# Optimization experiments

Hardware: AMD Instinct MI355X
Metric: run time of the kernel (lower is better)

Reference implementation:

```python
import jax, jax.numpy as jnp
import numpy as np

NUM_HEADS = 16
NUM_GQA_GROUPS = 4
HEAD_DIM = 128
TOTAL_TOKENS = 4096
NUM_SEQS = 8
SCALE = HEAD_DIM ** -0.5


def setup_inputs() -> dict:
    key = jax.random.key(0)
    kq, kk, kv, kc = jax.random.split(key, 4)
    query = jax.random.normal(kq, (TOTAL_TOKENS, NUM_HEADS, HEAD_DIM), dtype=jnp.float32)
    k = jax.random.normal(kk, (TOTAL_TOKENS, NUM_GQA_GROUPS, HEAD_DIM), dtype=jnp.float32)
    v = jax.random.normal(kv, (TOTAL_TOKENS, NUM_GQA_GROUPS, HEAD_DIM), dtype=jnp.float32)
    # cu_seqlens: sorted prefix boundaries, pinned to 0 and TOTAL_TOKENS
    inner = jnp.sort(jax.random.randint(kc, (NUM_SEQS - 1,), 1, TOTAL_TOKENS, dtype=jnp.int32))
    cu_seqlens = jnp.concatenate([
        jnp.zeros((1,), jnp.int32), inner,
        jnp.full((1,), TOTAL_TOKENS, jnp.int32)])
    return {"query": query, "key": k, "value": v, "cu_seqlens": cu_seqlens}


def reference(query, key, value, cu_seqlens):
    """Packed varlen (thd) causal attention with GQA, fused via a segment mask.

    query: [T, H, D]; key/value: [T, G, D]; cu_seqlens: [B+1] int32.
    Returns [T, H, D] (same layout the torch thd path concatenates back to).
    """
    T, H, D = query.shape
    ratio = H // key.shape[1]
    if ratio > 1:  # GQA: repeat kv heads to match query heads
        key = jnp.repeat(key, ratio, axis=1)
        value = jnp.repeat(value, ratio, axis=1)

    pos = jnp.arange(T, dtype=jnp.int32)
    # segment id of each packed token: cu[j] <= i < cu[j+1]
    seg = jnp.searchsorted(cu_seqlens, pos, side="right") - 1
    # within-segment causal mask (global causal == local causal inside a segment)
    mask = (seg[:, None] == seg[None, :]) & (pos[:, None] >= pos[None, :])  # [T, T]

    scores = jnp.einsum("qhd,khd->hqk", query, key) * SCALE  # [H, T, T]
    scores = jnp.where(mask[None], scores, -jnp.inf)
    probs = jax.nn.softmax(scores, axis=-1)
    out = jnp.einsum("hqk,khd->qhd", probs, value)  # [T, H, D]
    return out
```

## Files before the change

kernel.cpp:

```cpp
#include <hip/hip_runtime.h>
#include <hip/hip_bf16.h>


#define T_TOK 4096
#define NH    16
#define NG    4
#define HD    128
#define NCU   9
#define NTILE 128

#define ML_OFF  33554432l
#define Q_OFF   34078720l
#define KBF_OFF 34080776l
#define VTB_OFF 35129352l
#define QBF_OFF 36177928l
#define WS_END  40372232l

typedef short          short8_t __attribute__((ext_vector_type(8)));
typedef float          float4_t __attribute__((ext_vector_type(4)));
typedef unsigned int   uint2_t  __attribute__((ext_vector_type(2)));
typedef unsigned short ushort;

static __device__ inline unsigned pack2(float a, float b) {
    __hip_bfloat162 h = __float22bfloat162_rn(make_float2(a, b));
    union { __hip_bfloat162 h; unsigned u; } c; c.h = h;
    return c.u;
}
static __device__ inline short8_t cvt8(float4_t lo, float4_t hi) {
    union { unsigned u[4]; short8_t s; } r;
    r.u[0] = pack2(lo[0], lo[1]); r.u[1] = pack2(lo[2], lo[3]);
    r.u[2] = pack2(hi[0], hi[1]); r.u[3] = pack2(hi[2], hi[3]);
    return r.s;
}

#define NPQ 4194304l
#define NPK 1048576l
__global__ __launch_bounds__(256) void prep_cvt(
    const float* __restrict__ Q, const float* __restrict__ K,
    const float* __restrict__ V, float* __restrict__ WS)
{
    unsigned* Qb  = (unsigned*)(WS + QBF_OFF);
    unsigned* Kb  = (unsigned*)(WS + KBF_OFF);
    ushort*   Vtb = (ushort*)(WS + VTB_OFF);
    const int b = (int)blockIdx.x, tid = (int)threadIdx.x;
    if (b < 2048) {
        long p = (long)b * 256 + tid;
        const long stride = 2048l * 256;
        for (; p < NPQ + NPK; p += stride) {
            if (p < NPQ) {
                const float2 v = *(const float2*)&Q[2 * p];
                Qb[p] = pack2(v.x, v.y);
            } else {
                const float2 v = *(const float2*)&K[2 * (p - NPQ)];
                Kb[p - NPQ] = pack2(v.x, v.y);
            }
        }
    } else {
        const int bt  = b - 2048;
        const int g   = bt >> 8;
        const int rem = bt & 255;
        const int d0  = (rem >> 6) * 32;
        const int t0  = (rem & 63) * 64;
        __shared__ ushort tile[64][36];
        const int i2 = tid >> 3, jl = (tid & 7) * 4;
        #pragma unroll
        for (int ii = 0; ii < 2; ++ii) {
            const int t = t0 + i2 + ii * 32;
            const float4_t v = *(const float4_t*)&V[((long)t * NG + g) * HD + d0 + jl];
            *(unsigned*)&tile[i2 + ii * 32][jl]     = pack2(v[0], v[1]);
            *(unsigned*)&tile[i2 + ii * 32][jl + 2] = pack2(v[2], v[3]);
        }
        __syncthreads();
        const int jj = tid >> 3, tl = (tid & 7) * 8;
        union { ushort s[8]; short8_t v; } o;
        #pragma unroll
        for (int r = 0; r < 8; ++r) o.s[r] = tile[tl + r][jj];
        *(short8_t*)&Vtb[((long)(g * HD + d0 + jj)) * T_TOK + t0 + tl] = o.v;
    }
}

template <int MODE>
static __device__ __forceinline__ void attn_tile_body(
    const float* __restrict__ Q, const float* __restrict__ K,
    const float* __restrict__ V,
    const ushort* __restrict__ Qb, const ushort* __restrict__ Kb,
    const ushort* __restrict__ Vtb,
    const int* __restrict__ cu,
    float* __restrict__ O, float* __restrict__ WS,
    unsigned char* smem, int qtile, int g, int cz)
{
    constexpr bool CHUNKED = (MODE >= 1);
    constexpr bool BF      = (MODE == 2);

    ushort (*Ks)[32][136]   = (ushort (*)[32][136])smem;
    ushort (*Vt)[128][40]   = (ushort (*)[128][40])(smem + 17408);
    ushort (*pb)[2][16][40] = (ushort (*)[2][16][40])(smem + 37888);

    const int tid   = threadIdx.x;
    const int wave  = tid >> 6;
    const int split = wave >> 2;
    const int hw    = wave & 3;
    const int lane  = tid & 63;
    const int h     = g * 4 + hw;
    const int col   = lane & 15;
    const int quad  = lane >> 4;

    const int qbase = qtile * 32;
    const int qq[2] = { qbase + col, qbase + 16 + col };

    int seg_start[2] = {0, 0}, seg0 = 0;
    #pragma unroll
    for (int j = 1; j < NCU; ++j) {
        int cj = cu[j];
        if (cj <= qq[0])  seg_start[0] = cj;
        if (cj <= qq[1])  seg_start[1] = cj;
        if (cj <= qbase)  seg0         = cj;
    }
    const int k0       = seg0 & ~31;
    const int nblk_tot = (qbase + 32 - k0) >> 5;
    const int nc       = CHUNKED ? ((nblk_tot + 31) >> 5) : 1;
    if (CHUNKED && cz >= nc) return;
    int nblk = nblk_tot - (cz << 5);
    if (CHUNKED && nblk > 32) nblk = 32;
    const int nb0    = (nblk + 1) >> 1;
    const int kstart = k0 + (cz << 10) + split * nb0 * 32;

    const int smax[2] = { __shfl(seg_start[0], 15), __shfl(seg_start[1], 15) };

    short8_t qf[2][4];
    #pragma unroll
    for (int tt = 0; tt < 2; ++tt) {
        if constexpr (BF) {
            const ushort* qp = Qb + ((long)qq[tt] * NH + h) * HD + quad * 8;
            #pragma unroll
            for (int c = 0; c < 4; ++c)
                qf[tt][c] = *(const short8_t*)(qp + c * 32);
        } else {
            const float* qp = Q + ((long)qq[tt] * NH + h) * HD + quad * 8;
            #pragma unroll
            for (int c = 0; c < 4; ++c)
                qf[tt][c] = cvt8(*(const float4_t*)(qp + c * 32),
                                 *(const float4_t*)(qp + c * 32 + 4));
        }
    }

    float4_t oacc[2][8];
    #pragma unroll
    for (int tt = 0; tt < 2; ++tt)
        #pragma unroll
        for (int dt = 0; dt < 8; ++dt) oacc[tt][dt] = (float4_t){0.f, 0.f, 0.f, 0.f};

    float m_run[2] = {-10000.0f, -10000.0f};
    float l_run[2] = {0.0f, 0.0f};
    const float c_scale = 0.08838834764831845f * 1.4426950408889634f;

    const int stid = tid & 255;
    const int ki  = stid >> 3;
    const int ch  = (stid & 7) * 16;
    const int kp2 = (stid & 15) * 2;
    const int dc  = (stid >> 4) * 8;
    const int vd  = stid >> 1;
    const int vko = (stid & 1) * 16;

    float4_t kreg[4], vreg[4];
    short8_t krb[2], vrb[2];
    if constexpr (BF) {
        int key = kstart + ki; if (key > T_TOK - 1) key = T_TOK - 1;
        const ushort* kp = Kb + ((long)key * NG + g) * HD + ch;
        krb[0] = *(const short8_t*)kp; krb[1] = *(const short8_t*)(kp + 8);
        int ts = kstart + vko; if (ts > T_TOK - 16) ts = T_TOK - 16;
        const ushort* vp = Vtb + ((long)(g * HD + vd)) * T_TOK + ts;
        vrb[0] = *(const short8_t*)vp; vrb[1] = *(const short8_t*)(vp + 8);
    } else {
        int key = kstart + ki; if (key > T_TOK - 1) key = T_TOK - 1;
        const float* kp = K + ((long)key * NG + g) * HD + ch;
        kreg[0] = *(const float4_t*)kp;       kreg[1] = *(const float4_t*)(kp + 4);
        kreg[2] = *(const float4_t*)(kp + 8); kreg[3] = *(const float4_t*)(kp + 12);
        int key0 = kstart + kp2;     if (key0 > T_TOK - 1) key0 = T_TOK - 1;
        int key1 = kstart + kp2 + 1; if (key1 > T_TOK - 1) key1 = T_TOK - 1;
        const float* v0 = V + ((long)key0 * NG + g) * HD + dc;
        const float* v1 = V + ((long)key1 * NG + g) * HD + dc;
        vreg[0] = *(const float4_t*)v0; vreg[1] = *(const float4_t*)(v0 + 4);
        vreg[2] = *(const float4_t*)v1; vreg[3] = *(const float4_t*)(v1 + 4);
    }

    for (int it = 0; it < nb0; ++it) {
        const int kb = kstart + it * 32;
        __syncthreads();

        if constexpr (BF) {
            *(short8_t*)&Ks[split][ki][ch]      = krb[0];
            *(short8_t*)&Ks[split][ki][ch + 8]  = krb[1];
            *(short8_t*)&Vt[split][vd][vko]     = vrb[0];
            *(short8_t*)&Vt[split][vd][vko + 8] = vrb[1];
        } else {
            *(short8_t*)&Ks[split][ki][ch]     = cvt8(kreg[0], kreg[1]);
            *(short8_t*)&Ks[split][ki][ch + 8] = cvt8(kreg[2], kreg[3]);
            #pragma unroll
            for (int d = 0; d < 4; ++d) {
                *(unsigned*)&Vt[split][dc + d][kp2]     = pack2(vreg[0][d], vreg[2][d]);
                *(unsigned*)&Vt[split][dc + 4 + d][kp2] = pack2(vreg[1][d], vreg[3][d]);
            }
        }
        __syncthreads();

        {
            int nb = kb + 32;
            if constexpr (BF) {
                int key = nb + ki; if (key > T_TOK - 1) key = T_TOK - 1;
                const ushort* kp = Kb + ((long)key * NG + g) * HD + ch;
                krb[0] = *(const short8_t*)kp; krb[1] = *(const short8_t*)(kp + 8);
                int ts = nb + vko; if (ts > T_TOK - 16) ts = T_TOK - 16;
                const ushort* vp = Vtb + ((long)(g * HD + vd)) * T_TOK + ts;
                vrb[0] = *(const short8_t*)vp; vrb[1] = *(const short8_t*)(vp + 8);
            } else {
                int key = nb + ki; if (key > T_TOK - 1) key = T_TOK - 1;
                const float* kp = K + ((long)key * NG + g) * HD + ch;
                kreg[0] = *(const float4_t*)kp;       kreg[1] = *(const float4_t*)(kp + 4);
                kreg[2] = *(const float4_t*)(kp + 8); kreg[3] = *(const float4_t*)(kp + 12);
                int key0 = nb + kp2;     if (key0 > T_TOK - 1) key0 = T_TOK - 1;
                int key1 = nb + kp2 + 1; if (key1 > T_TOK - 1) key1 = T_TOK - 1;
                const float* v0 = V + ((long)key0 * NG + g) * HD + dc;
                const float* v1 = V + ((long)key1 * NG + g) * HD + dc;
                vreg[0] = *(const float4_t*)v0; vreg[1] = *(const float4_t*)(v0 + 4);
                vreg[2] = *(const float4_t*)v1; vreg[3] = *(const float4_t*)(v1 + 4);
            }
        }

        float4_t st[2][2];
        #pragma unroll
        for (int tt = 0; tt < 2; ++tt)
            #pragma unroll
            for (int t = 0; t < 2; ++t) st[tt][t] = (float4_t){0.f, 0.f, 0.f, 0.f};
        #pragma unroll
        for (int c = 0; c < 4; ++c) {
            short8_t kf0 = *(const short8_t*)&Ks[split][col][c * 32 + quad * 8];
            short8_t kf1 = *(const short8_t*)&Ks[split][16 + col][c * 32 + quad * 8];
            st[0][0] = __builtin_amdgcn_mfma_f32_16x16x32_bf16(kf0, qf[0][c], st[0][0], 0, 0, 0);
            st[0][1] = __builtin_amdgcn_mfma_f32_16x16x32_bf16(kf1, qf[0][c], st[0][1], 0, 0, 0);
            st[1][0] = __builtin_amdgcn_mfma_f32_16x16x32_bf16(kf0, qf[1][c], st[1][0], 0, 0, 0);
            st[1][1] = __builtin_amdgcn_mfma_f32_16x16x32_bf16(kf1, qf[1][c], st[1][1], 0, 0, 0);
        }

        #pragma unroll
        for (int tt = 0; tt < 2; ++tt) {
            float tv[8];
            if (kb + 31 <= qbase + 16 * tt && kb >= smax[tt]) {
                #pragma unroll
                for (int i = 0; i < 8; ++i)
                    tv[i] = st[tt][i >> 2][i & 3] * c_scale;
            } else {
                #pragma unroll
                for (int t = 0; t < 2; ++t)
                    #pragma unroll
                    for (int r = 0; r < 4; ++r) {
                        int key = kb + 16 * t + quad * 4 + r;
                        bool valid = (key <= qq[tt]) && (key >= seg_start[tt]);
                        tv[t * 4 + r] = valid ? st[tt][t][r] * c_scale : -30000.0f;
                    }
            }
            float tmax = tv[0];
            #pragma unroll
            for (int i = 1; i < 8; ++i) tmax = fmaxf(tmax, tv[i]);
            tmax = fmaxf(tmax, __shfl_xor(tmax, 16));
            tmax = fmaxf(tmax, __shfl_xor(tmax, 32));
            const float m_new = fmaxf(m_run[tt], tmax);
            float p[8], ps = 0.f;
            #pragma unroll
            for (int i = 0; i < 8; ++i) { p[i] = __builtin_exp2f(tv[i] - m_new); ps += p[i]; }
            ps += __shfl_xor(ps, 16);
            ps += __shfl_xor(ps, 32);
            if (__any(tmax > m_run[tt])) {
                const float alpha = __builtin_exp2f(m_run[tt] - m_new);
                l_run[tt] = l_run[tt] * alpha + ps;
                m_run[tt] = m_new;
                #pragma unroll
                for (int dt = 0; dt < 8; ++dt) oacc[tt][dt] *= alpha;
            } else {
                l_run[tt] += ps;
            }

            uint2_t w0; w0.x = pack2(p[0], p[1]); w0.y = pack2(p[2], p[3]);
            uint2_t w1; w1.x = pack2(p[4], p[5]); w1.y = pack2(p[6], p[7]);
            *(uint2_t*)&pb[wave][tt][col][quad * 4]      = w0;
            *(uint2_t*)&pb[wave][tt][col][16 + quad * 4] = w1;
        }
        short8_t pf0 = *(const short8_t*)&pb[wave][0][col][quad * 8];
        short8_t pf1 = *(const short8_t*)&pb[wave][1][col][quad * 8];

        #pragma unroll
        for (int dt = 0; dt < 8; ++dt) {
            short8_t vf = *(const short8_t*)&Vt[split][dt * 16 + col][quad * 8];
            oacc[0][dt] = __builtin_amdgcn_mfma_f32_16x16x32_bf16(vf, pf0, oacc[0][dt], 0, 0, 0);
            oacc[1][dt] = __builtin_amdgcn_mfma_f32_16x16x32_bf16(vf, pf1, oacc[1][dt], 0, 0, 0);
        }
    }

    float* Ob = (float*)smem;
    float* cm = (float*)(smem + 34816);
    float* cl = (float*)(smem + 35840);
    #pragma unroll
    for (int tt = 0; tt < 2; ++tt) {
        __syncthreads();
        if (split == 1) {
            if (quad == 0) { cm[hw * 16 + col] = m_run[tt]; cl[hw * 16 + col] = l_run[tt]; }
            float* ob = Ob + (hw * 16 + col) * 132;
            #pragma unroll
            for (int dt = 0; dt < 8; ++dt)
                *(float4_t*)(ob + dt * 16 + quad * 4) = oacc[tt][dt];
        }
        __syncthreads();
        if (split == 0) {
            const float m1 = cm[hw * 16 + col], l1 = cl[hw * 16 + col];
            const float m  = fmaxf(m_run[tt], m1);
            const float a0 = __builtin_exp2f(m_run[tt] - m);
            const float a1 = __builtin_exp2f(m1 - m);
            const float* ob = Ob + (hw * 16 + col) * 132;
            #pragma unroll
            for (int dt = 0; dt < 8; ++dt) {
                float4_t o1 = *(const float4_t*)(ob + dt * 16 + quad * 4);
                oacc[tt][dt] = oacc[tt][dt] * a0 + o1 * a1;
            }
            l_run[tt] = l_run[tt] * a0 + l1 * a1;
            m_run[tt] = m;
        }
    }

    if (split == 0) {
        if (!CHUNKED || nc == 1) {
            #pragma unroll
            for (int tt = 0; tt < 2; ++tt) {
                const float inv_l = 1.0f / l_run[tt];
                float* op = O + ((long)qq[tt] * NH + h) * HD + quad * 4;
                #pragma unroll
                for (int dt = 0; dt < 8; ++dt) {
                    float4_t ov;
                    #pragma unroll
                    for (int r = 0; r < 4; ++r) ov[r] = oacc[tt][dt][r] * inv_l;
                    *(float4_t*)(op + dt * 16) = ov;
                }
            }
        } else {
            const long slot = ((long)(qtile * 4 + g)) * 4 + cz;
            #pragma unroll
            for (int tt = 0; tt < 2; ++tt) {
                const int ql = tt * 16 + col;
                if (quad == 0) {
                    float* mlp = WS + ML_OFF + (slot * 128 + hw * 32 + ql) * 2;
                    mlp[0] = m_run[tt];
                    mlp[1] = l_run[tt];
                }
                float* op = WS + (slot * 128 + hw * 32 + ql) * 128 + quad * 4;
                #pragma unroll
                for (int dt = 0; dt < 8; ++dt)
                    *(float4_t*)(op + dt * 16) = oacc[tt][dt];
            }
        }
    }
}

__global__ __launch_bounds__(128) void build_queue(
    const int* __restrict__ cu, int* __restrict__ qwork)
{
    __shared__ int nblk_s[NTILE];
    __shared__ int sortedE[NTILE + 1];
    const int t = threadIdx.x;

    const int qbase = t * 32;
    int seg0 = 0;
    #pragma unroll
    for (int j = 1; j < NCU; ++j) { int cj = cu[j]; if (cj <= qbase) seg0 = cj; }
    const int k0   = seg0 & ~31;
    const int nblk = (qbase + 32 - k0) >> 5;
    nblk_s[t] = nblk;
    __syncthreads();

    int r = 0;
    for (int j = 0; j < NTILE; ++j) {
        int nj = nblk_s[j];
        if (nj > nblk || (nj == nblk && j < t)) ++r;
    }
    const int nc = (nblk + 31) >> 5;
    sortedE[r] = 4 * nc;
    __syncthreads();
    if (t == 0) {
        int s = 0;
        for (int j = 0; j < NTILE; ++j) { int v = sortedE[j]; sortedE[j] = s; s += v; }
        sortedE[NTILE] = s;
        qwork[0] = s;
        qwork[1] = 0;
    }
    __syncthreads();
    int off = 2 + sortedE[r];
    for (int g = 0; g < NG; ++g)
        for (int cz = 0; cz < nc; ++cz)
            qwork[off++] = (t << 4) | (g << 2) | cz;
}

template <int MODE>
__global__ __launch_bounds__(512) void attn_fwd_persist(
    const float* __restrict__ Q,
    const float* __restrict__ K,
    const float* __restrict__ V,
    const int*   __restrict__ cu,
    float*       __restrict__ O,
    float*       __restrict__ WS)
{
    __shared__ __align__(16) unsigned char smem[58368];
    __shared__ int pop_s;
    int* qwork = (int*)(WS + Q_OFF);
    const ushort* Qb  = (const ushort*)(WS + QBF_OFF);
    const ushort* Kb  = (const ushort*)(WS + KBF_OFF);
    const ushort* Vtb = (const ushort*)(WS + VTB_OFF);
    const int qtotal = qwork[0];

    for (;;) {
        __syncthreads();
        if (threadIdx.x == 0) pop_s = atomicAdd(&qwork[1], 1);
        __syncthreads();
        const int idx = pop_s;
        if (idx >= qtotal) return;
        const int ent = qwork[2 + idx];
        attn_tile_body<MODE>(Q, K, V, Qb, Kb, Vtb, cu, O, WS, smem,
                             ent >> 4, (ent >> 2) & 3, ent & 3);
    }
}

__global__ __launch_bounds__(512) void attn_fwd_mono(
    const float* __restrict__ Q,
    const float* __restrict__ K,
    const float* __restrict__ V,
    const int*   __restrict__ cu,
    float*       __restrict__ O)
{
    __shared__ __align__(16) unsigned char smem[58368];
    attn_tile_body<0>(Q, K, V, nullptr, nullptr, nullptr, cu, O, nullptr, smem,
                      (int)gridDim.x - 1 - (int)blockIdx.x,
                      (int)blockIdx.y, 0);
}

__global__ __launch_bounds__(256) void attn_merge(
    const int*   __restrict__ cu,
    const float* __restrict__ WS,
    float*       __restrict__ O)
{
    const int tile  = blockIdx.x;
    const int g     = blockIdx.y;
    const int qbase = tile * 32;
    int seg0 = 0;
    #pragma unroll
    for (int j = 1; j < NCU; ++j) { int cj = cu[j]; if (cj <= qbase) seg0 = cj; }
    const int k0       = seg0 & ~31;
    const int nblk_tot = (qbase + 32 - k0) >> 5;
    const int nc       = (nblk_tot + 31) >> 5;
    if (nc <= 1) return;

    const int tid  = threadIdx.x;
    const int pair = tid >> 1;
    const int half = tid & 1;
    const int hw   = pair >> 5;
    const int q    = pair & 31;

    float m = -30000.0f, l = 0.0f;
    float4_t acc[16];
    #pragma unroll
    for (int i = 0; i < 16; ++i) acc[i] = (float4_t){0.f, 0.f, 0.f, 0.f};

    for (int c = 0; c < nc; ++c) {
        const long slot = ((long)(tile * 4 + g)) * 4 + c;
        const float* mlp = WS + ML_OFF + (slot * 128 + pair) * 2;
        const float mc = mlp[0], lc = mlp[1];
        const float mn = fmaxf(m, mc);
        const float a0 = __builtin_exp2f(m - mn);
        const float a1 = __builtin_exp2f(mc - mn);
        l = l * a0 + lc * a1;
        const float* op = WS + (slot * 128 + pair) * 128 + half * 64;
        #pragma unroll
        for (int i = 0; i < 16; ++i) {
            float4_t v = *(const float4_t*)(op + i * 4);
            acc[i] = acc[i] * a0 + v * a1;
        }
        m = mn;
    }
    const float inv = 1.0f / l;
    float* o = O + ((long)(qbase + q) * NH + g * 4 + hw) * HD + half * 64;
    #pragma unroll
    for (int i = 0; i < 16; ++i)
        *(float4_t*)(o + i * 4) = acc[i] * inv;
}

extern "C" void kernel_launch(void* const* d_in, const int* in_sizes, int n_in,
                              void* d_out, int out_size, void* d_ws, size_t ws_size,
                              hipStream_t stream) {
    const float* Q  = (const float*)d_in[0];
    const float* K  = (const float*)d_in[1];
    const float* V  = (const float*)d_in[2];
    const int*   cu = (const int*)d_in[3];
    float*       O  = (float*)d_out;
    const size_t need_bf  = (size_t)WS_END * sizeof(float);
    const size_t need_f32 = (size_t)(33554432l + 524288l + 2056l) * sizeof(float);
    if (d_ws != nullptr && ws_size >= need_bf) {
        float* WS = (float*)d_ws;
        prep_cvt<<<3072, 256, 0, stream>>>(Q, K, V, WS);
        build_queue<<<1, 128, 0, stream>>>(cu, (int*)(WS + Q_OFF));
        attn_fwd_persist<2><<<512, 512, 0, stream>>>(Q, K, V, cu, O, WS);
        attn_merge<<<dim3(T_TOK / 32, NG), 256, 0, stream>>>(
            cu, (const float*)WS, O);
    } else if (d_ws != nullptr && ws_size >= need_f32) {
        float* WS = (float*)d_ws;
        build_queue<<<1, 128, 0, stream>>>(cu, (int*)(WS + Q_OFF));
        attn_fwd_persist<1><<<512, 512, 0, stream>>>(Q, K, V, cu, O, WS);
        attn_merge<<<dim3(T_TOK / 32, NG), 256, 0, stream>>>(
            cu, (const float*)WS, O);
    } else {
        attn_fwd_mono<<<dim3(T_TOK / 32, NG), 512, 0, stream>>>(Q, K, V, cu, O);
    }
}
```

Baseline: 187.5 us.

## Fuse split-KV merge into attention via atomic last-chunk reduction, finer KV splits

Removes the separate merge kernel: each chunk writes partial output as bf16 plus m/l stats, bumps an atomic counter, and the last-arriving chunk does the log-sum-exp merge in place. Splitting changes from fixed 32-block chunks to up to 8 balanced chunks of about 12 blocks each, for better load balance across the persistent grid. Query bf16 pre-conversion is dropped (Q is converted on load), and queue building and counter reset are folded into a single prep kernel alongside the K/V conversion. This cuts launches and workspace traffic, at the cost of extra atomics and fences, bf16 rounding of partial outputs, and more merge work from the larger number of chunks.

After: 494.4 us. 164% more time.

```diff
diff --git a/kernel.cpp b/kernel.cpp
--- a/kernel.cpp
+++ b/kernel.cpp
@@ -10,11 +10,11 @@
 #define NTILE 128
 
 #define ML_OFF  33554432l
-#define Q_OFF   34078720l
-#define KBF_OFF 34080776l
-#define VTB_OFF 35129352l
-#define QBF_OFF 36177928l
-#define WS_END  40372232l
+#define Q_OFF   34603008l
+#define CNT_OFF 34607108l
+#define KBF_OFF 34607620l
+#define VTB_OFF 35656196l
+#define WS_END  36704772l
 
 typedef short          short8_t __attribute__((ext_vector_type(8)));
 typedef float          float4_t __attribute__((ext_vector_type(4)));
@@ -32,31 +32,29 @@
     r.u[2] = pack2(hi[0], hi[1]); r.u[3] = pack2(hi[2], hi[3]);
     return r.s;
 }
-
-#define NPQ 4194304l
+static __device__ inline float bf2f(ushort u) {
+    union { unsigned i; float f; } c; c.i = ((unsigned)u) << 16; return c.f;
+}
+static __device__ __forceinline__ int nc_of(int nblk) {
+    int nc = (nblk + 11) / 12;
+    return nc < 1 ? 1 : (nc > 8 ? 8 : nc);
+}
+
 #define NPK 1048576l
-__global__ __launch_bounds__(256) void prep_cvt(
-    const float* __restrict__ Q, const float* __restrict__ K,
-    const float* __restrict__ V, float* __restrict__ WS)
+__global__ __launch_bounds__(256) void prep_all(
+    const float* __restrict__ K, const float* __restrict__ V,
+    const int* __restrict__ cu, float* __restrict__ WS)
 {
-    unsigned* Qb  = (unsigned*)(WS + QBF_OFF);
-    unsigned* Kb  = (unsigned*)(WS + KBF_OFF);
-    ushort*   Vtb = (ushort*)(WS + VTB_OFF);
     const int b = (int)blockIdx.x, tid = (int)threadIdx.x;
-    if (b < 2048) {
-        long p = (long)b * 256 + tid;
-        const long stride = 2048l * 256;
-        for (; p < NPQ + NPK; p += stride) {
-            if (p < NPQ) {
-                const float2 v = *(const float2*)&Q[2 * p];
-                Qb[p] = pack2(v.x, v.y);
-            } else {
-                const float2 v = *(const float2*)&K[2 * (p - NPQ)];
-                Kb[p - NPQ] = pack2(v.x, v.y);
-            }
-        }
-    } else {
-        const int bt  = b - 2048;
+    if (b < 512) {
+        unsigned* Kb = (unsigned*)(WS + KBF_OFF);
+        for (long p = (long)b * 256 + tid; p < NPK; p += 512l * 256) {
+            const float2 v = *(const float2*)&K[2 * p];
+            Kb[p] = pack2(v.x, v.y);
+        }
+    } else if (b < 1536) {
+        ushort* Vtb = (ushort*)(WS + VTB_OFF);
+        const int bt  = b - 512;
         const int g   = bt >> 8;
         const int rem = bt & 255;
         const int d0  = (rem >> 6) * 32;
@@ -76,22 +74,56 @@
         #pragma unroll
         for (int r = 0; r < 8; ++r) o.s[r] = tile[tl + r][jj];
         *(short8_t*)&Vtb[((long)(g * HD + d0 + jj)) * T_TOK + t0 + tl] = o.v;
-    }
-}
-
-template <int MODE>
+    } else {
+        int* qwork = (int*)(WS + Q_OFF);
+        int* cnt   = (int*)(WS + CNT_OFF);
+        __shared__ int nblk_s[NTILE];
+        __shared__ int sortedE[NTILE + 1];
+        if (tid >= 128) {
+            for (int i = tid - 128; i < 512; i += 128) cnt[i] = 0;
+            return;
+        }
+        const int t = tid;
+        const int qbase = t * 32;
+        int seg0 = 0;
+        #pragma unroll
+        for (int j = 1; j < NCU; ++j) { int cj = cu[j]; if (cj <= qbase) seg0 = cj; }
+        const int k0   = seg0 & ~31;
+        const int nblk = (qbase + 32 - k0) >> 5;
+        nblk_s[t] = nblk;
+        __syncthreads();
+        int r = 0;
+        for (int j = 0; j < NTILE; ++j) {
+            int nj = nblk_s[j];
+            if (nj > nblk || (nj == nblk && j < t)) ++r;
+        }
+        const int nc = nc_of(nblk);
+        sortedE[r] = 4 * nc;
+        __syncthreads();
+        if (t == 0) {
+            int s = 0;
+            for (int j = 0; j < NTILE; ++j) { int v = sortedE[j]; sortedE[j] = s; s += v; }
+            sortedE[NTILE] = s;
+            qwork[0] = s;
+            qwork[1] = 0;
+        }
+        __syncthreads();
+        int off = 2 + sortedE[r];
+        for (int g = 0; g < NG; ++g)
+            for (int cz = 0; cz < nc; ++cz)
+                qwork[off++] = (t << 5) | (g << 3) | cz;
+    }
+}
+
+template <bool CHB>
 static __device__ __forceinline__ void attn_tile_body(
     const float* __restrict__ Q, const float* __restrict__ K,
     const float* __restrict__ V,
-    const ushort* __restrict__ Qb, const ushort* __restrict__ Kb,
-    const ushort* __restrict__ Vtb,
+    const ushort* __restrict__ Kb, const ushort* __restrict__ Vtb,
     const int* __restrict__ cu,
     float* __restrict__ O, float* __restrict__ WS,
     unsigned char* smem, int qtile, int g, int cz)
 {
-    constexpr bool CHUNKED = (MODE >= 1);
-    constexpr bool BF      = (MODE == 2);
-
     ushort (*Ks)[32][136]   = (ushort (*)[32][136])smem;
     ushort (*Vt)[128][40]   = (ushort (*)[128][40])(smem + 17408);
     ushort (*pb)[2][16][40] = (ushort (*)[2][16][40])(smem + 37888);
@@ -118,30 +150,29 @@
     }
     const int k0       = seg0 & ~31;
     const int nblk_tot = (qbase + 32 - k0) >> 5;
-    const int nc       = CHUNKED ? ((nblk_tot + 31) >> 5) : 1;
-    if (CHUNKED && cz >= nc) return;
-    int nblk = nblk_tot - (cz << 5);
-    if (CHUNKED && nblk > 32) nblk = 32;
+
+    int nc = 1, kb_lo = 0, nblk = nblk_tot;
+    if (CHB) {
+        nc = nc_of(nblk_tot);
+        int chunk = ((nblk_tot + nc - 1) / nc + 1) & ~1;
+        kb_lo = cz * chunk;
+        nblk  = nblk_tot - kb_lo;
+        if (nblk > chunk) nblk = chunk;
+        if (nblk < 1) return;
+    }
     const int nb0    = (nblk + 1) >> 1;
-    const int kstart = k0 + (cz << 10) + split * nb0 * 32;
+    const int kstart = k0 + (kb_lo + split * nb0) * 32;
 
     const int smax[2] = { __shfl(seg_start[0], 15), __shfl(seg_start[1], 15) };
 
     short8_t qf[2][4];
     #pragma unroll
     for (int tt = 0; tt < 2; ++tt) {
-        if constexpr (BF) {
-            const ushort* qp = Qb + ((long)qq[tt] * NH + h) * HD + quad * 8;
-            #pragma unroll
-            for (int c = 0; c < 4; ++c)
-                qf[tt][c] = *(const short8_t*)(qp + c * 32);
-        } else {
-            const float* qp = Q + ((long)qq[tt] * NH + h) * HD + quad * 8;
-            #pragma unroll
-            for (int c = 0; c < 4; ++c)
-                qf[tt][c] = cvt8(*(const float4_t*)(qp + c * 32),
-                                 *(const float4_t*)(qp + c * 32 + 4));
-        }
+        const float* qp = Q + ((long)qq[tt] * NH + h) * HD + quad * 8;
+        #pragma unroll
+        for (int c = 0; c < 4; ++c)
+            qf[tt][c] = cvt8(*(const float4_t*)(qp + c * 32),
+                             *(const float4_t*)(qp + c * 32 + 4));
     }
 
     float4_t oacc[2][8];
@@ -164,7 +195,7 @@
 
     float4_t kreg[4], vreg[4];
     short8_t krb[2], vrb[2];
-    if constexpr (BF) {
+    if constexpr (CHB) {
         int key = kstart + ki; if (key > T_TOK - 1) key = T_TOK - 1;
         const ushort* kp = Kb + ((long)key * NG + g) * HD + ch;
         krb[0] = *(const short8_t*)kp; krb[1] = *(const short8_t*)(kp + 8);
@@ -188,7 +219,7 @@
         const int kb = kstart + it * 32;
         __syncthreads();
 
-        if constexpr (BF) {
+        if constexpr (CHB) {
             *(short8_t*)&Ks[split][ki][ch]      = krb[0];
             *(short8_t*)&Ks[split][ki][ch + 8]  = krb[1];
             *(short8_t*)&Vt[split][vd][vko]     = vrb[0];
@@ -206,7 +237,7 @@
 
         {
             int nb = kb + 32;
-            if constexpr (BF) {
+            if constexpr (CHB) {
                 int key = nb + ki; if (key > T_TOK - 1) key = T_TOK - 1;
                 const ushort* kp = Kb + ((long)key * NG + g) * HD + ch;
                 krb[0] = *(const short8_t*)kp; krb[1] = *(const short8_t*)(kp + 8);
@@ -326,8 +357,8 @@
         }
     }
 
-    if (split == 0) {
-        if (!CHUNKED || nc == 1) {
+    if (!CHB || nc == 1) {
+        if (split == 0) {
             #pragma unroll
             for (int tt = 0; tt < 2; ++tt) {
                 const float inv_l = 1.0f / l_run[tt];
@@ -340,64 +371,78 @@
                     *(float4_t*)(op + dt * 16) = ov;
                 }
             }
-        } else {
-            const long slot = ((long)(qtile * 4 + g)) * 4 + cz;
-            #pragma unroll
-            for (int tt = 0; tt < 2; ++tt) {
-                const int ql = tt * 16 + col;
-                if (quad == 0) {
-                    float* mlp = WS + ML_OFF + (slot * 128 + hw * 32 + ql) * 2;
-                    mlp[0] = m_run[tt];
-                    mlp[1] = l_run[tt];
-                }
-                float* op = WS + (slot * 128 + hw * 32 + ql) * 128 + quad * 4;
-                #pragma unroll
-                for (int dt = 0; dt < 8; ++dt)
-                    *(float4_t*)(op + dt * 16) = oacc[tt][dt];
-            }
-        }
-    }
-}
-
-__global__ __launch_bounds__(128) void build_queue(
-    const int* __restrict__ cu, int* __restrict__ qwork)
-{
-    __shared__ int nblk_s[NTILE];
-    __shared__ int sortedE[NTILE + 1];
-    const int t = threadIdx.x;
-
-    const int qbase = t * 32;
-    int seg0 = 0;
-    #pragma unroll
-    for (int j = 1; j < NCU; ++j) { int cj = cu[j]; if (cj <= qbase) seg0 = cj; }
-    const int k0   = seg0 & ~31;
-    const int nblk = (qbase + 32 - k0) >> 5;
-    nblk_s[t] = nblk;
+        }
+        return;
+    }
+
+    const long slot = ((long)(qtile * 4 + g)) * 8 + cz;
+    if (split == 0) {
+        ushort* ob = (ushort*)WS + slot * 16384;
+        #pragma unroll
+        for (int tt = 0; tt < 2; ++tt) {
+            const int row = hw * 32 + tt * 16 + col;
+            if (quad == 0) {
+                float* mlp = WS + ML_OFF + slot * 256 + row * 2;
+                mlp[0] = m_run[tt];
+                mlp[1] = l_run[tt];
+            }
+            ushort* op = ob + row * 128 + quad * 4;
+            #pragma unroll
+            for (int dt = 0; dt < 8; ++dt) {
+                uint2_t w;
+                w.x = pack2(oacc[tt][dt][0], oacc[tt][dt][1]);
+                w.y = pack2(oacc[tt][dt][2], oacc[tt][dt][3]);
+                *(uint2_t*)(op + dt * 16) = w;
+            }
+        }
+    }
+
+    __threadfence();
     __syncthreads();
-
-    int r = 0;
-    for (int j = 0; j < NTILE; ++j) {
-        int nj = nblk_s[j];
-        if (nj > nblk || (nj == nblk && j < t)) ++r;
-    }
-    const int nc = (nblk + 31) >> 5;
-    sortedE[r] = 4 * nc;
+    int* flag = (int*)(smem + 37888);
+    if (tid == 0) {
+        int* cnt = (int*)(WS + CNT_OFF);
+        *flag = atomicAdd(&cnt[qtile * 4 + g], 1);
+    }
     __syncthreads();
-    if (t == 0) {
-        int s = 0;
-        for (int j = 0; j < NTILE; ++j) { int v = sortedE[j]; sortedE[j] = s; s += v; }
-        sortedE[NTILE] = s;
-        qwork[0] = s;
-        qwork[1] = 0;
-    }
-    __syncthreads();
-    int off = 2 + sortedE[r];
-    for (int g = 0; g < NG; ++g)
-        for (int cz = 0; cz < nc; ++cz)
-            qwork[off++] = (t << 4) | (g << 2) | cz;
-}
-
-template <int MODE>
+    const bool last = (*flag == nc - 1);
+    if (!last) return;
+    __threadfence();
+
+    {
+        const int row  = tid >> 2;
+        const int dseg = (tid & 3) * 32;
+        float m = -30000.0f, l = 0.0f;
+        float4_t acc[8];
+        #pragma unroll
+        for (int i = 0; i < 8; ++i) acc[i] = (float4_t){0.f, 0.f, 0.f, 0.f};
+        const long sbase = ((long)(qtile * 4 + g)) * 8;
+        for (int c = 0; c < nc; ++c) {
+            const float* mlp = WS + ML_OFF + (sbase + c) * 256 + row * 2;
+            const float mc = mlp[0], lc = mlp[1];
+            const float mn = fmaxf(m, mc);
+            const float a0 = __builtin_exp2f(m - mn);
+            const float a1 = __builtin_exp2f(mc - mn);
+            l = l * a0 + lc * a1;
+            const ushort* op = (const ushort*)WS + (sbase + c) * 16384 + row * 128 + dseg;
+            #pragma unroll
+            for (int i = 0; i < 8; ++i) {
+                float4_t v;
+                v[0] = bf2f(op[i * 4 + 0]); v[1] = bf2f(op[i * 4 + 1]);
+                v[2] = bf2f(op[i * 4 + 2]); v[3] = bf2f(op[i * 4 + 3]);
+                acc[i] = acc[i] * a0 + v * a1;
+            }
+            m = mn;
+        }
+        const float inv = 1.0f / l;
+        const int q = row & 31, hwm = row >> 5;
+        float* o = O + ((long)(qbase + q) * NH + g * 4 + hwm) * HD + dseg;
+        #pragma unroll
+        for (int i = 0; i < 8; ++i)
+            *(float4_t*)(o + i * 4) = acc[i] * inv;
+    }
+}
+
 __global__ __launch_bounds__(512) void attn_fwd_persist(
     const float* __restrict__ Q,
     const float* __restrict__ K,
@@ -409,7 +454,6 @@
     __shared__ __align__(16) unsigned char smem[58368];
     __shared__ int pop_s;
     int* qwork = (int*)(WS + Q_OFF);
-    const ushort* Qb  = (const ushort*)(WS + QBF_OFF);
     const ushort* Kb  = (const ushort*)(WS + KBF_OFF);
     const ushort* Vtb = (const ushort*)(WS + VTB_OFF);
     const int qtotal = qwork[0];
@@ -421,8 +465,8 @@
         const int idx = pop_s;
         if (idx >= qtotal) return;
         const int ent = qwork[2 + idx];
-        attn_tile_body<MODE>(Q, K, V, Qb, Kb, Vtb, cu, O, WS, smem,
-                             ent >> 4, (ent >> 2) & 3, ent & 3);
+        attn_tile_body<true>(Q, K, V, Kb, Vtb, cu, O, WS, smem,
+                             ent >> 5, (ent >> 3) & 3, ent & 7);
     }
 }
 
@@ -434,59 +478,9 @@
     float*       __restrict__ O)
 {
     __shared__ __align__(16) unsigned char smem[58368];
-    attn_tile_body<0>(Q, K, V, nullptr, nullptr, nullptr, cu, O, nullptr, smem,
-                      (int)gridDim.x - 1 - (int)blockIdx.x,
-                      (int)blockIdx.y, 0);
-}
-
-__global__ __launch_bounds__(256) void attn_merge(
-    const int*   __restrict__ cu,
-    const float* __restrict__ WS,
-    float*       __restrict__ O)
-{
-    const int tile  = blockIdx.x;
-    const int g     = blockIdx.y;
-    const int qbase = tile * 32;
-    int seg0 = 0;
-    #pragma unroll
-    for (int j = 1; j < NCU; ++j) { int cj = cu[j]; if (cj <= qbase) seg0 = cj; }
-    const int k0       = seg0 & ~31;
-    const int nblk_tot = (qbase + 32 - k0) >> 5;
-    const int nc       = (nblk_tot + 31) >> 5;
-    if (nc <= 1) return;
-
-    const int tid  = threadIdx.x;
-    const int pair = tid >> 1;
-    const int half = tid & 1;
-    const int hw   = pair >> 5;
-    const int q    = pair & 31;
-
-    float m = -30000.0f, l = 0.0f;
-    float4_t acc[16];
-    #pragma unroll
-    for (int i = 0; i < 16; ++i) acc[i] = (float4_t){0.f, 0.f, 0.f, 0.f};
-
-    for (int c = 0; c < nc; ++c) {
-        const long slot = ((long)(tile * 4 + g)) * 4 + c;
-        const float* mlp = WS + ML_OFF + (slot * 128 + pair) * 2;
-        const float mc = mlp[0], lc = mlp[1];
-        const float mn = fmaxf(m, mc);
-        const float a0 = __builtin_exp2f(m - mn);
-        const float a1 = __builtin_exp2f(mc - mn);
-        l = l * a0 + lc * a1;
-        const float* op = WS + (slot * 128 + pair) * 128 + half * 64;
-        #pragma unroll
-        for (int i = 0; i < 16; ++i) {
-            float4_t v = *(const float4_t*)(op + i * 4);
-            acc[i] = acc[i] * a0 + v * a1;
-        }
-        m = mn;
-    }
-    const float inv = 1.0f / l;
-    float* o = O + ((long)(qbase + q) * NH + g * 4 + hw) * HD + half * 64;
-    #pragma unroll
-    for (int i = 0; i < 16; ++i)
-        *(float4_t*)(o + i * 4) = acc[i] * inv;
+    attn_tile_body<false>(Q, K, V, nullptr, nullptr, cu, O, nullptr, smem,
+                          (int)gridDim.x - 1 - (int)blockIdx.x,
+                          (int)blockIdx.y, 0);
 }
 
 extern "C" void kernel_launch(void* const* d_in, const int* in_sizes, int n_in,
@@ -497,21 +491,11 @@
     const float* V  = (const float*)d_in[2];
     const int*   cu = (const int*)d_in[3];
     float*       O  = (float*)d_out;
-    const size_t need_bf  = (size_t)WS_END * sizeof(float);
-    const size_t need_f32 = (size_t)(33554432l + 524288l + 2056l) * sizeof(float);
-    if (d_ws != nullptr && ws_size >= need_bf) {
+    const size_t need = (size_t)WS_END * sizeof(float);
+    if (d_ws != nullptr && ws_size >= need) {
         float* WS = (float*)d_ws;
-        prep_cvt<<<3072, 256, 0, stream>>>(Q, K, V, WS);
-        build_queue<<<1, 128, 0, stream>>>(cu, (int*)(WS + Q_OFF));
-        attn_fwd_persist<2><<<512, 512, 0, stream>>>(Q, K, V, cu, O, WS);
-        attn_merge<<<dim3(T_TOK / 32, NG), 256, 0, stream>>>(
-            cu, (const float*)WS, O);
-    } else if (d_ws != nullptr && ws_size >= need_f32) {
-        float* WS = (float*)d_ws;
-        build_queue<<<1, 128, 0, stream>>>(cu, (int*)(WS + Q_OFF));
-        attn_fwd_persist<1><<<512, 512, 0, stream>>>(Q, K, V, cu, O, WS);
-        attn_merge<<<dim3(T_TOK / 32, NG), 256, 0, stream>>>(
-            cu, (const float*)WS, O);
+        prep_all<<<1537, 256, 0, stream>>>(K, V, cu, WS);
+        attn_fwd_persist<<<512, 512, 0, stream>>>(Q, K, V, cu, O, WS);
     } else {
         attn_fwd_mono<<<dim3(T_TOK / 32, NG), 512, 0, stream>>>(Q, K, V, cu, O);
     }
```
